# Performance work log

Hardware: AMD Instinct MI355X
Metric: run time of the kernel (lower is better)

Reference implementation:

```python
import jax, jax.numpy as jnp
import numpy as np

N = 100000      # nodes
E = 1600000     # edges (avg degree 16)
F_IN = 128      # num_node_features
H = 64          # hidden_features
C = 40          # num_classes


def _glorot(key, shape):
    lim = np.sqrt(6.0 / (shape[0] + shape[1]))
    return jax.random.uniform(key, shape, jnp.float32, -lim, lim)


def setup_inputs() -> dict:
    key = jax.random.key(0)
    k = jax.random.split(key, 4)
    x = jax.random.normal(k[0], (N, F_IN), dtype=jnp.float32)
    edge_index = jax.random.randint(k[1], (2, E), 0, N, dtype=jnp.int32)
    W1 = _glorot(k[2], (F_IN, H))
    b1 = jnp.zeros((H,), jnp.float32)
    W2 = _glorot(k[3], (H, C))
    b2 = jnp.zeros((C,), jnp.float32)
    return {"x": x, "edge_index": edge_index, "W1": W1, "b1": b1, "W2": W2, "b2": b2}


def _gcn_conv(x, src, dst, dinv_sqrt, W, b):
    # GCNConv: out = D^{-1/2} (A + I) D^{-1/2} (x W) + b
    h = x @ W                                        # [N, out]
    norm = dinv_sqrt[src] * dinv_sqrt[dst]           # [E+N]
    msg = h[src] * norm[:, None]                     # gather + scale
    agg = jax.ops.segment_sum(msg, dst, num_segments=N)
    return agg + b


def reference(x, edge_index, W1, b1, W2, b2):
    loop = jnp.arange(N, dtype=edge_index.dtype)
    src = jnp.concatenate([edge_index[0], loop])     # add self-loops
    dst = jnp.concatenate([edge_index[1], loop])
    # degree of A + I (counts in-edges at destination, incl. self-loop)
    deg = jax.ops.segment_sum(jnp.ones_like(dst, jnp.float32), dst, num_segments=N)
    dinv_sqrt = jax.lax.rsqrt(deg)                   # deg >= 1 due to self-loops

    h = _gcn_conv(x, src, dst, dinv_sqrt, W1, b1)
    h = jax.nn.relu(h)
    # F.dropout(training=self.training) is identity in eval mode
    out = _gcn_conv(h, src, dst, dinv_sqrt, W2, b2)
    return out
```

## Files before the change

### kernel.cpp

```cpp
#include <hip/hip_runtime.h>
#include <hip/hip_fp16.h>
#include <cstdint>
#include <cstddef>

#define NPB_SHIFT 8
#define NPB (1 << NPB_SHIFT)
#define CHUNK 4096
#define BCHUNK 8192

typedef _Float16 half8_t __attribute__((ext_vector_type(8)));
typedef _Float16 half4_t __attribute__((ext_vector_type(4)));
typedef _Float16 half2_t __attribute__((ext_vector_type(2)));
typedef float floatx4 __attribute__((ext_vector_type(4)));

#define H2(u) __builtin_bit_cast(half2_t, (u))


__global__ __launch_bounds__(256) void k_bcount(const int* __restrict__ dst,
                                                int* __restrict__ btot, int E, int nbuck) {
  __shared__ int cnt[512];
  int tid = threadIdx.x;
  for (int i = tid; i < nbuck; i += 256) cnt[i] = 0;
  __syncthreads();
  int base = blockIdx.x * BCHUNK;
  int end = min(base + BCHUNK, E);
  for (int e = base + tid; e < end; e += 256) atomicAdd(&cnt[dst[e] >> NPB_SHIFT], 1);
  __syncthreads();
  for (int i = tid; i < nbuck; i += 256)
    if (cnt[i]) atomicAdd(&btot[i], cnt[i]);
}

__global__ void k_bscan(const int* __restrict__ btot, int* __restrict__ bbase,
                        int* __restrict__ bfill, int nbuck, int E) {
  __shared__ int tmp[512];
  int tid = threadIdx.x;
  int v = (tid < nbuck) ? btot[tid] : 0;
  tmp[tid] = v;
  __syncthreads();
  for (int off = 1; off < 512; off <<= 1) {
    int t = (tid >= off) ? tmp[tid - off] : 0;
    __syncthreads();
    tmp[tid] += t;
    __syncthreads();
  }
  if (tid < nbuck) { int ex = tmp[tid] - v; bbase[tid] = ex; bfill[tid] = ex; }
  if (tid == 0) bbase[nbuck] = E;
}

__global__ __launch_bounds__(256) void k_partition(const int* __restrict__ src,
                                                   const int* __restrict__ dst,
                                                   int* __restrict__ bfill,
                                                   unsigned* __restrict__ tmp,
                                                   int E, int nbuck) {
  __shared__ int cnt[512];
  __shared__ int lbase[512];
  __shared__ int gdelta[512];
  __shared__ int cur[512];
  __shared__ int ps[256];
  __shared__ unsigned sval[CHUNK];
  __shared__ unsigned short sbid[CHUNK];
  int tid = threadIdx.x;
  int cbase = blockIdx.x * CHUNK;
  for (int i = tid; i < 512; i += 256) cnt[i] = 0;
  __syncthreads();
  int s[16], d[16];
  bool valid[16];
#pragma unroll
  for (int u = 0; u < 16; ++u) {
    int e = cbase + u * 256 + tid;
    valid[u] = e < E;
    s[u] = valid[u] ? src[e] : 0;
    d[u] = valid[u] ? dst[e] : 0;
    if (valid[u]) atomicAdd(&cnt[d[u] >> NPB_SHIFT], 1);
  }
  __syncthreads();
  int c0 = cnt[2 * tid], c1 = cnt[2 * tid + 1];
  int p = c0 + c1;
  ps[tid] = p;
  __syncthreads();
  for (int off = 1; off < 256; off <<= 1) {
    int t = (tid >= off) ? ps[tid - off] : 0;
    __syncthreads();
    ps[tid] += t;
    __syncthreads();
  }
  int ep = ps[tid] - p;
  lbase[2 * tid] = ep;
  lbase[2 * tid + 1] = ep + c0;
  __syncthreads();
  for (int i = tid; i < 512; i += 256) {
    cur[i] = lbase[i];
    if (cnt[i]) gdelta[i] = atomicAdd(&bfill[i], cnt[i]) - lbase[i];
  }
  __syncthreads();
#pragma unroll
  for (int u = 0; u < 16; ++u) {
    if (valid[u]) {
      int b = d[u] >> NPB_SHIFT;
      int r = atomicAdd(&cur[b], 1);
      sval[r] = ((unsigned)s[u] << NPB_SHIFT) | (unsigned)(d[u] & (NPB - 1));
      sbid[r] = (unsigned short)b;
    }
  }
  __syncthreads();
  int nv = min(CHUNK, E - cbase);
  for (int i = tid; i < nv; i += 256) {
    unsigned v = sval[i];
    int b = sbid[i];
    tmp[gdelta[b] + i] = v;
  }
}

__global__ __launch_bounds__(256) void k_csr_build(const unsigned* __restrict__ tmp,
                                                   const int* __restrict__ bbase,
                                                   float* __restrict__ dinv,
                                                   int* __restrict__ offset,
                                                   int* __restrict__ ssrc,
                                                   int N, int E, int nbuck) {
  __shared__ int cnt[NPB];
  __shared__ int scan[NPB];
  __shared__ int fillL[NPB];
  int b = blockIdx.x, tid = threadIdx.x;
  int nbase = b << NPB_SHIFT;
  int nloc = min(NPB, N - nbase);
  cnt[tid] = 0;
  __syncthreads();
  int ebeg = bbase[b], eend = bbase[b + 1];
  for (int j = ebeg + tid; j < eend; j += 256) atomicAdd(&cnt[tmp[j] & (NPB - 1)], 1);
  __syncthreads();
  int v = cnt[tid];
  scan[tid] = v;
  __syncthreads();
  for (int off = 1; off < NPB; off <<= 1) {
    int t = (tid >= off) ? scan[tid - off] : 0;
    __syncthreads();
    scan[tid] += t;
    __syncthreads();
  }
  int myoff = ebeg + scan[tid] - v;
  fillL[tid] = myoff;
  if (tid < nloc) {
    offset[nbase + tid] = myoff;
    dinv[nbase + tid] = rsqrtf((float)(v + 1));
  }
  if (b == nbuck - 1 && tid == 0) offset[N] = E;
  __syncthreads();
  int j = ebeg + tid;
  for (; j + 3 * 256 < eend; j += 4 * 256) {
    unsigned p[4];
#pragma unroll
    for (int u = 0; u < 4; ++u) p[u] = tmp[j + u * 256];
#pragma unroll
    for (int u = 0; u < 4; ++u) {
      int pos = atomicAdd(&fillL[p[u] & (NPB - 1)], 1);
      ssrc[pos] = (int)(p[u] >> NPB_SHIFT);
    }
  }
  for (; j < eend; j += 256) {
    unsigned p = tmp[j];
    int pos = atomicAdd(&fillL[p & (NPB - 1)], 1);
    ssrc[pos] = (int)(p >> NPB_SHIFT);
  }
}

template <int K, int COLS, int MT, int KC, int OS>
__global__ __launch_bounds__(256) void k_gemm_mfma(const float* __restrict__ x,
                                                   const float* __restrict__ W,
                                                   const float* __restrict__ dinv,
                                                   _Float16* __restrict__ out, int n) {
  int lane = threadIdx.x & 63;
  int quad = lane >> 4;
  int l15 = lane & 15;
  int gwave = (blockIdx.x * blockDim.x + threadIdx.x) >> 6;
  int nwave = (gridDim.x * blockDim.x) >> 6;
  int ntiles = (n + 15) >> 4;

  half8_t afrag[MT][KC];
#pragma unroll
  for (int m = 0; m < MT; ++m) {
    int colw = m * 16 + l15;
    if (colw > COLS - 1) colw = COLS - 1;
#pragma unroll
    for (int c = 0; c < KC; ++c) {
#pragma unroll
      for (int j = 0; j < 8; ++j) {
        int kk = c * 32 + quad * 8 + j;
        afrag[m][c][j] = (_Float16)W[kk * COLS + colw];
      }
    }
  }

  for (int tile = gwave; tile < ntiles; tile += nwave) {
    int node0 = tile << 4;
    int nodeB = node0 + l15;
    int nodeC = nodeB < n ? nodeB : n - 1;
    const float* xr = x + (size_t)nodeC * K;
    float dv = dinv[nodeC];
    half8_t bfrag[KC];
#pragma unroll
    for (int c = 0; c < KC; ++c) {
      float4 lo = *(const float4*)(xr + c * 32 + quad * 8);
      float4 hi = *(const float4*)(xr + c * 32 + quad * 8 + 4);
      bfrag[c][0] = (_Float16)lo.x; bfrag[c][1] = (_Float16)lo.y;
      bfrag[c][2] = (_Float16)lo.z; bfrag[c][3] = (_Float16)lo.w;
      bfrag[c][4] = (_Float16)hi.x; bfrag[c][5] = (_Float16)hi.y;
      bfrag[c][6] = (_Float16)hi.z; bfrag[c][7] = (_Float16)hi.w;
    }
    floatx4 acc[MT];
#pragma unroll
    for (int m = 0; m < MT; ++m) acc[m] = (floatx4){0.f, 0.f, 0.f, 0.f};
#pragma unroll
    for (int c = 0; c < KC; ++c)
#pragma unroll
      for (int m = 0; m < MT; ++m)
        acc[m] = __builtin_amdgcn_mfma_f32_16x16x32_f16(afrag[m][c], bfrag[c], acc[m], 0, 0, 0);

    if (nodeB < n) {
#pragma unroll
      for (int m = 0; m < MT; ++m) {
        int colBase = m * 16 + quad * 4;
        if (colBase < COLS) {
          half4_t hv = {(_Float16)(acc[m][0] * dv), (_Float16)(acc[m][1] * dv),
                        (_Float16)(acc[m][2] * dv), (_Float16)(acc[m][3] * dv)};
          *(half4_t*)(out + (size_t)nodeB * OS + colBase) = hv;
        }
      }
    }
  }
}

template <int F, int S8, bool RELU>
__global__ __launch_bounds__(256) void k_agg_v8(const uint4* __restrict__ h8,
                                                const int* __restrict__ offset,
                                                const int* __restrict__ ssrc,
                                                const float* __restrict__ dinv,
                                                const float* __restrict__ bias,
                                                float* __restrict__ outp, int n) {
  constexpr int F8 = F / 8;
  int lane = threadIdx.x & 63;
  int g = lane >> 3;
  int t = lane & 7;
  int node = (blockIdx.x * blockDim.x + threadIdx.x) >> 6;
  if (node >= n) return;
  bool tv = t < F8;
  float di = dinv[node];
  half2_t acc[4];
#pragma unroll
  for (int k = 0; k < 4; ++k) acc[k] = H2(0u);

  if (g == 0 && tv) {
    uint4 v = h8[(size_t)node * S8 + t];
    acc[0] += H2(v.x); acc[1] += H2(v.y); acc[2] += H2(v.z); acc[3] += H2(v.w);
  }

  int beg = offset[node], end = offset[node + 1];
  int j = beg;
  for (; j + 16 <= end; j += 16) {
    int sA = ssrc[j + g];
    int sB = ssrc[j + 8 + g];
    uint4 rA = tv ? h8[(size_t)sA * S8 + t] : make_uint4(0, 0, 0, 0);
    uint4 rB = tv ? h8[(size_t)sB * S8 + t] : make_uint4(0, 0, 0, 0);
    acc[0] += H2(rA.x); acc[1] += H2(rA.y); acc[2] += H2(rA.z); acc[3] += H2(rA.w);
    acc[0] += H2(rB.x); acc[1] += H2(rB.y); acc[2] += H2(rB.z); acc[3] += H2(rB.w);
  }
  for (; j + 8 <= end; j += 8) {
    int s = ssrc[j + g];
    uint4 rv = tv ? h8[(size_t)s * S8 + t] : make_uint4(0, 0, 0, 0);
    acc[0] += H2(rv.x); acc[1] += H2(rv.y); acc[2] += H2(rv.z); acc[3] += H2(rv.w);
  }
  if (j < end) {
    int r = end - j;
    int gi = (g < r) ? g : (r - 1);
    int s = ssrc[j + gi];
    uint4 rv = (tv && g < r) ? h8[(size_t)s * S8 + t] : make_uint4(0, 0, 0, 0);
    acc[0] += H2(rv.x); acc[1] += H2(rv.y); acc[2] += H2(rv.z); acc[3] += H2(rv.w);
  }

#pragma unroll
  for (int k = 0; k < 4; ++k) {
    int u = __builtin_bit_cast(int, acc[k]);
    acc[k] += H2((unsigned)__shfl_xor(u, 8));
    u = __builtin_bit_cast(int, acc[k]);
    acc[k] += H2((unsigned)__shfl_xor(u, 16));
    u = __builtin_bit_cast(int, acc[k]);
    acc[k] += H2((unsigned)__shfl_xor(u, 32));
  }

  if (lane < F8) {
    float f[8];
#pragma unroll
    for (int k = 0; k < 4; ++k) {
      f[2 * k] = (float)acc[k][0];
      f[2 * k + 1] = (float)acc[k][1];
    }
    const float* bb = bias + lane * 8;
    float4 r0 = make_float4(fmaf(f[0], di, bb[0]), fmaf(f[1], di, bb[1]),
                            fmaf(f[2], di, bb[2]), fmaf(f[3], di, bb[3]));
    float4 r1 = make_float4(fmaf(f[4], di, bb[4]), fmaf(f[5], di, bb[5]),
                            fmaf(f[6], di, bb[6]), fmaf(f[7], di, bb[7]));
    if (RELU) {
      r0.x = fmaxf(r0.x, 0.f); r0.y = fmaxf(r0.y, 0.f);
      r0.z = fmaxf(r0.z, 0.f); r0.w = fmaxf(r0.w, 0.f);
      r1.x = fmaxf(r1.x, 0.f); r1.y = fmaxf(r1.y, 0.f);
      r1.z = fmaxf(r1.z, 0.f); r1.w = fmaxf(r1.w, 0.f);
    }
    float4* o4 = (float4*)(outp + (size_t)node * F + lane * 8);
    o4[0] = r0; o4[1] = r1;
  }
}


extern "C" void kernel_launch(void* const* d_in, const int* in_sizes, int n_in,
                              void* d_out, int out_size, void* d_ws, size_t ws_size,
                              hipStream_t stream) {
  const float* x  = (const float*)d_in[0];
  const int*   ei = (const int*)d_in[1];
  const float* W1 = (const float*)d_in[2];
  const float* b1 = (const float*)d_in[3];
  const float* W2 = (const float*)d_in[4];
  const float* b2 = (const float*)d_in[5];
  float* out = (float*)d_out;

  const int F_IN = 128, HID = 64, C = 40;
  int N = in_sizes[0] / F_IN;
  int E = in_sizes[1] / 2;
  const int* src = ei;
  const int* dst = ei + E;
  int nbuck = (N + NPB - 1) >> NPB_SHIFT;

  char* w = (char*)d_ws;
  size_t o = 0;
  auto alloc = [&](size_t bytes) -> void* {
    void* p = w + o;
    o = (o + bytes + 255) & ~(size_t)255;
    return p;
  };
  float*    dinv   = (float*)alloc((size_t)N * 4);
  int*      offset = (int*)alloc((size_t)(N + 1) * 4);
  int*      btot   = (int*)alloc(512 * 4);
  int*      bbase  = (int*)alloc(513 * 4);
  int*      bfill  = (int*)alloc(512 * 4);
  unsigned* tmp    = (unsigned*)alloc((size_t)E * 4);
  int*      ssrc   = (int*)alloc((size_t)E * 4);
  _Float16* g1     = (_Float16*)alloc((size_t)N * HID * 2);
  float*    h1     = (float*)alloc((size_t)N * HID * 4);
  _Float16* g2     = (_Float16*)alloc((size_t)N * C * 2);

  dim3 b256(256);

  hipMemsetAsync(btot, 0, 512 * 4, stream);
  k_bcount<<<dim3((E + BCHUNK - 1) / BCHUNK), b256, 0, stream>>>(dst, btot, E, nbuck);
  k_bscan<<<dim3(1), dim3(512), 0, stream>>>(btot, bbase, bfill, nbuck, E);

  k_partition<<<dim3((E + CHUNK - 1) / CHUNK), b256, 0, stream>>>(src, dst, bfill, tmp, E, nbuck);
  k_csr_build<<<dim3(nbuck), b256, 0, stream>>>(tmp, bbase, dinv, offset, ssrc, N, E, nbuck);

  k_gemm_mfma<128, 64, 4, 4, 64><<<dim3(256), b256, 0, stream>>>(x, W1, dinv, g1, N);
  k_agg_v8<64, 8, true><<<dim3((N + 3) / 4), b256, 0, stream>>>(
      (const uint4*)g1, offset, ssrc, dinv, b1, h1, N);

  k_gemm_mfma<64, 40, 3, 2, 40><<<dim3(256), b256, 0, stream>>>(h1, W2, dinv, g2, N);
  k_agg_v8<40, 5, false><<<dim3((N + 3) / 4), b256, 0, stream>>>(
      (const uint4*)g2, offset, ssrc, dinv, b2, out, N);
}
```

Baseline: 265.4 us.

## Process four nodes per wave in aggregation and store hidden layer as fp16

The aggregation kernel now gives each wave four destination nodes and interleaves their neighbor gathers, so more independent loads are in flight per wave and less time is spent waiting on latency. The first layer's hidden output is written as fp16 instead of fp32, and the second GEMM reads it directly as half8 fragments. This halves that intermediate's write and read traffic and removes the conversion in the GEMM. In exchange there is extra fp16 rounding after ReLU, and wave divergence when degrees differ among the four nodes.

```diff
diff --git a/kernel.cpp b/kernel.cpp
--- a/kernel.cpp
+++ b/kernel.cpp
@@ -163,8 +163,8 @@
   }
 }
 
-template <int K, int COLS, int MT, int KC, int OS>
-__global__ __launch_bounds__(256) void k_gemm_mfma(const float* __restrict__ x,
+template <int K, int COLS, int MT, int KC, int OS, typename XT>
+__global__ __launch_bounds__(256) void k_gemm_mfma(const XT* __restrict__ x,
                                                    const float* __restrict__ W,
                                                    const float* __restrict__ dinv,
                                                    _Float16* __restrict__ out, int n) {
@@ -194,17 +194,21 @@
     int node0 = tile << 4;
     int nodeB = node0 + l15;
     int nodeC = nodeB < n ? nodeB : n - 1;
-    const float* xr = x + (size_t)nodeC * K;
+    const XT* xr = x + (size_t)nodeC * K;
     float dv = dinv[nodeC];
     half8_t bfrag[KC];
 #pragma unroll
     for (int c = 0; c < KC; ++c) {
-      float4 lo = *(const float4*)(xr + c * 32 + quad * 8);
-      float4 hi = *(const float4*)(xr + c * 32 + quad * 8 + 4);
-      bfrag[c][0] = (_Float16)lo.x; bfrag[c][1] = (_Float16)lo.y;
-      bfrag[c][2] = (_Float16)lo.z; bfrag[c][3] = (_Float16)lo.w;
-      bfrag[c][4] = (_Float16)hi.x; bfrag[c][5] = (_Float16)hi.y;
-      bfrag[c][6] = (_Float16)hi.z; bfrag[c][7] = (_Float16)hi.w;
+      if constexpr (sizeof(XT) == 4) {
+        float4 lo = *(const float4*)(xr + c * 32 + quad * 8);
+        float4 hi = *(const float4*)(xr + c * 32 + quad * 8 + 4);
+        bfrag[c][0] = (_Float16)lo.x; bfrag[c][1] = (_Float16)lo.y;
+        bfrag[c][2] = (_Float16)lo.z; bfrag[c][3] = (_Float16)lo.w;
+        bfrag[c][4] = (_Float16)hi.x; bfrag[c][5] = (_Float16)hi.y;
+        bfrag[c][6] = (_Float16)hi.z; bfrag[c][7] = (_Float16)hi.w;
+      } else {
+        bfrag[c] = *(const half8_t*)(xr + c * 32 + quad * 8);
+      }
     }
     floatx4 acc[MT];
 #pragma unroll
@@ -229,83 +233,146 @@
   }
 }
 
-template <int F, int S8, bool RELU>
-__global__ __launch_bounds__(256) void k_agg_v8(const uint4* __restrict__ h8,
+
+__device__ __forceinline__ void addacc(half2_t* acc, uint4 r) {
+  acc[0] += H2(r.x); acc[1] += H2(r.y); acc[2] += H2(r.z); acc[3] += H2(r.w);
+}
+
+template <int F, int S8, bool RELU, bool OUT_HALF>
+__global__ __launch_bounds__(256) void k_agg_v4(const uint4* __restrict__ g8,
                                                 const int* __restrict__ offset,
                                                 const int* __restrict__ ssrc,
                                                 const float* __restrict__ dinv,
                                                 const float* __restrict__ bias,
-                                                float* __restrict__ outp, int n) {
+                                                void* __restrict__ outp, int n) {
   constexpr int F8 = F / 8;
   int lane = threadIdx.x & 63;
   int g = lane >> 3;
   int t = lane & 7;
-  int node = (blockIdx.x * blockDim.x + threadIdx.x) >> 6;
-  if (node >= n) return;
+  int wave = (blockIdx.x * blockDim.x + threadIdx.x) >> 6;
+  int nb = wave * 4;
+  if (nb >= n) return;
   bool tv = t < F8;
-  float di = dinv[node];
-  half2_t acc[4];
-#pragma unroll
-  for (int k = 0; k < 4; ++k) acc[k] = H2(0u);
-
-  if (g == 0 && tv) {
-    uint4 v = h8[(size_t)node * S8 + t];
-    acc[0] += H2(v.x); acc[1] += H2(v.y); acc[2] += H2(v.z); acc[3] += H2(v.w);
-  }
-
-  int beg = offset[node], end = offset[node + 1];
-  int j = beg;
-  for (; j + 16 <= end; j += 16) {
-    int sA = ssrc[j + g];
-    int sB = ssrc[j + 8 + g];
-    uint4 rA = tv ? h8[(size_t)sA * S8 + t] : make_uint4(0, 0, 0, 0);
-    uint4 rB = tv ? h8[(size_t)sB * S8 + t] : make_uint4(0, 0, 0, 0);
-    acc[0] += H2(rA.x); acc[1] += H2(rA.y); acc[2] += H2(rA.z); acc[3] += H2(rA.w);
-    acc[0] += H2(rB.x); acc[1] += H2(rB.y); acc[2] += H2(rB.z); acc[3] += H2(rB.w);
-  }
-  for (; j + 8 <= end; j += 8) {
-    int s = ssrc[j + g];
-    uint4 rv = tv ? h8[(size_t)s * S8 + t] : make_uint4(0, 0, 0, 0);
-    acc[0] += H2(rv.x); acc[1] += H2(rv.y); acc[2] += H2(rv.z); acc[3] += H2(rv.w);
-  }
-  if (j < end) {
-    int r = end - j;
-    int gi = (g < r) ? g : (r - 1);
-    int s = ssrc[j + gi];
-    uint4 rv = (tv && g < r) ? h8[(size_t)s * S8 + t] : make_uint4(0, 0, 0, 0);
-    acc[0] += H2(rv.x); acc[1] += H2(rv.y); acc[2] += H2(rv.z); acc[3] += H2(rv.w);
-  }
-
-#pragma unroll
-  for (int k = 0; k < 4; ++k) {
-    int u = __builtin_bit_cast(int, acc[k]);
-    acc[k] += H2((unsigned)__shfl_xor(u, 8));
-    u = __builtin_bit_cast(int, acc[k]);
-    acc[k] += H2((unsigned)__shfl_xor(u, 16));
-    u = __builtin_bit_cast(int, acc[k]);
-    acc[k] += H2((unsigned)__shfl_xor(u, 32));
-  }
-
-  if (lane < F8) {
-    float f[8];
+
+  uint4 sv[4];
+#pragma unroll
+  for (int w = 0; w < 4; ++w) {
+    int node = nb + w;
+    int nc = node < n ? node : n - 1;
+    sv[w] = (tv && g == 0 && node < n) ? g8[(size_t)nc * S8 + t]
+                                       : make_uint4(0, 0, 0, 0);
+  }
+
+  int jj[4], ee[4];
+  float di[4];
+#pragma unroll
+  for (int w = 0; w < 4; ++w) {
+    int node = nb + w;
+    bool nv = node < n;
+    int nc = nv ? node : n - 1;
+    int b0 = offset[nc];
+    int b1 = offset[nc + 1];
+    jj[w] = b0;
+    ee[w] = nv ? b1 : b0;
+    di[w] = dinv[nc];
+  }
+
+  half2_t acc[4][4];
+#pragma unroll
+  for (int w = 0; w < 4; ++w) {
+#pragma unroll
+    for (int k = 0; k < 4; ++k) acc[w][k] = H2(0u);
+    addacc(acc[w], sv[w]);
+  }
+
+  for (;;) {
+    bool a0[4], a1[4];
+    bool any = false;
+#pragma unroll
+    for (int w = 0; w < 4; ++w) {
+      a0[w] = jj[w] + 8 <= ee[w];
+      a1[w] = jj[w] + 16 <= ee[w];
+      any = any || a0[w];
+    }
+    if (!any) break;
+    int s0[4], s1[4];
+#pragma unroll
+    for (int w = 0; w < 4; ++w) {
+      s0[w] = a0[w] ? ssrc[jj[w] + g] : 0;
+      s1[w] = a1[w] ? ssrc[jj[w] + 8 + g] : 0;
+    }
+    uint4 r0[4], r1[4];
+#pragma unroll
+    for (int w = 0; w < 4; ++w) {
+      r0[w] = (a0[w] && tv) ? g8[(size_t)s0[w] * S8 + t] : make_uint4(0, 0, 0, 0);
+      r1[w] = (a1[w] && tv) ? g8[(size_t)s1[w] * S8 + t] : make_uint4(0, 0, 0, 0);
+    }
+#pragma unroll
+    for (int w = 0; w < 4; ++w) {
+      addacc(acc[w], r0[w]);
+      addacc(acc[w], r1[w]);
+      jj[w] += a1[w] ? 16 : (a0[w] ? 8 : 0);
+    }
+  }
+
+  {
+    int rem[4];
+    uint4 rv[4];
+#pragma unroll
+    for (int w = 0; w < 4; ++w) {
+      rem[w] = ee[w] - jj[w];
+      int gi = (g < rem[w]) ? g : (rem[w] - 1);
+      int sW = rem[w] > 0 ? ssrc[jj[w] + gi] : 0;
+      rv[w] = (tv && g < rem[w]) ? g8[(size_t)sW * S8 + t] : make_uint4(0, 0, 0, 0);
+    }
+#pragma unroll
+    for (int w = 0; w < 4; ++w) addacc(acc[w], rv[w]);
+  }
+
+#pragma unroll
+  for (int w = 0; w < 4; ++w) {
 #pragma unroll
     for (int k = 0; k < 4; ++k) {
-      f[2 * k] = (float)acc[k][0];
-      f[2 * k + 1] = (float)acc[k][1];
-    }
-    const float* bb = bias + lane * 8;
-    float4 r0 = make_float4(fmaf(f[0], di, bb[0]), fmaf(f[1], di, bb[1]),
-                            fmaf(f[2], di, bb[2]), fmaf(f[3], di, bb[3]));
-    float4 r1 = make_float4(fmaf(f[4], di, bb[4]), fmaf(f[5], di, bb[5]),
-                            fmaf(f[6], di, bb[6]), fmaf(f[7], di, bb[7]));
-    if (RELU) {
-      r0.x = fmaxf(r0.x, 0.f); r0.y = fmaxf(r0.y, 0.f);
-      r0.z = fmaxf(r0.z, 0.f); r0.w = fmaxf(r0.w, 0.f);
-      r1.x = fmaxf(r1.x, 0.f); r1.y = fmaxf(r1.y, 0.f);
-      r1.z = fmaxf(r1.z, 0.f); r1.w = fmaxf(r1.w, 0.f);
-    }
-    float4* o4 = (float4*)(outp + (size_t)node * F + lane * 8);
-    o4[0] = r0; o4[1] = r1;
+      int u = __builtin_bit_cast(int, acc[w][k]);
+      acc[w][k] += H2((unsigned)__shfl_xor(u, 8));
+      u = __builtin_bit_cast(int, acc[w][k]);
+      acc[w][k] += H2((unsigned)__shfl_xor(u, 16));
+      u = __builtin_bit_cast(int, acc[w][k]);
+      acc[w][k] += H2((unsigned)__shfl_xor(u, 32));
+    }
+    int node = nb + w;
+    if (node < n && lane < F8) {
+      float f[8];
+#pragma unroll
+      for (int k = 0; k < 4; ++k) {
+        f[2 * k] = (float)acc[w][k][0];
+        f[2 * k + 1] = (float)acc[w][k][1];
+      }
+      const float* bb = bias + lane * 8;
+      float o[8];
+#pragma unroll
+      for (int j = 0; j < 8; ++j) {
+        o[j] = fmaf(f[j], di[w], bb[j]);
+        if (RELU) o[j] = fmaxf(o[j], 0.f);
+      }
+      if (OUT_HALF) {
+        _Float16* op = (_Float16*)outp + (size_t)node * F + lane * 8;
+        half2_t p0 = {(_Float16)o[0], (_Float16)o[1]};
+        half2_t p1 = {(_Float16)o[2], (_Float16)o[3]};
+        half2_t p2 = {(_Float16)o[4], (_Float16)o[5]};
+        half2_t p3 = {(_Float16)o[6], (_Float16)o[7]};
+        uint4 wv;
+        wv.x = __builtin_bit_cast(unsigned, p0);
+        wv.y = __builtin_bit_cast(unsigned, p1);
+        wv.z = __builtin_bit_cast(unsigned, p2);
+        wv.w = __builtin_bit_cast(unsigned, p3);
+        *(uint4*)op = wv;
+      } else {
+        float* op = (float*)outp + (size_t)node * F + lane * 8;
+        *(float4*)op = make_float4(o[0], o[1], o[2], o[3]);
+        *(float4*)(op + 4) = make_float4(o[4], o[5], o[6], o[7]);
+      }
+    }
   }
 }
 
@@ -343,7 +410,7 @@
   unsigned* tmp    = (unsigned*)alloc((size_t)E * 4);
   int*      ssrc   = (int*)alloc((size_t)E * 4);
   _Float16* g1     = (_Float16*)alloc((size_t)N * HID * 2);
-  float*    h1     = (float*)alloc((size_t)N * HID * 4);
+  _Float16* h1     = (_Float16*)alloc((size_t)N * HID * 2);
   _Float16* g2     = (_Float16*)alloc((size_t)N * C * 2);
 
   dim3 b256(256);
@@ -355,11 +422,11 @@
   k_partition<<<dim3((E + CHUNK - 1) / CHUNK), b256, 0, stream>>>(src, dst, bfill, tmp, E, nbuck);
   k_csr_build<<<dim3(nbuck), b256, 0, stream>>>(tmp, bbase, dinv, offset, ssrc, N, E, nbuck);
 
-  k_gemm_mfma<128, 64, 4, 4, 64><<<dim3(256), b256, 0, stream>>>(x, W1, dinv, g1, N);
-  k_agg_v8<64, 8, true><<<dim3((N + 3) / 4), b256, 0, stream>>>(
+  k_gemm_mfma<128, 64, 4, 4, 64, float><<<dim3(256), b256, 0, stream>>>(x, W1, dinv, g1, N);
+  k_agg_v4<64, 8, true, true><<<dim3((N + 15) / 16), b256, 0, stream>>>(
       (const uint4*)g1, offset, ssrc, dinv, b1, h1, N);
 
-  k_gemm_mfma<64, 40, 3, 2, 40><<<dim3(256), b256, 0, stream>>>(h1, W2, dinv, g2, N);
-  k_agg_v8<40, 5, false><<<dim3((N + 3) / 4), b256, 0, stream>>>(
+  k_gemm_mfma<64, 40, 3, 2, 40, _Float16><<<dim3(256), b256, 0, stream>>>(h1, W2, dinv, g2, N);
+  k_agg_v4<40, 5, false, false><<<dim3((N + 15) / 16), b256, 0, stream>>>(
       (const uint4*)g2, offset, ssrc, dinv, b2, out, N);
 }
```

New measurement: 264.1 us. No clear change (-0.5%).
